# Kernel optimization log

Hardware: AMD Instinct MI355X
Metric: run time of the kernel (lower is better)

## Reference

```python
import jax, jax.numpy as jnp
import numpy as np

B, H, W, C, FD, HID = 64, 128, 128, 10, 32, 64
OFFSETS = [(-1,-1),(-1,0),(-1,1),(0,-1),(0,1),(1,-1),(1,0),(1,1)]

def setup_inputs() -> dict:
    key = jax.random.key(0)
    ks = jax.random.split(key, 13)
    s = lambda n: 1.0 / np.sqrt(n)
    return {
        "beliefs": jax.random.normal(ks[0], (B, H, W, C), jnp.float32),
        "constraints": jax.random.uniform(ks[1], (B, H, W, 8, 3), jnp.float32),
        "filename_embed": jax.random.normal(ks[2], (B, FD), jnp.float32),
        # message_net: Linear(2C+3+FD -> HID), ReLU, Linear(HID -> C)
        "mw1": jax.random.uniform(ks[3], (2*C+3+FD, HID), jnp.float32, -s(2*C+3+FD), s(2*C+3+FD)),
        "mb1": jax.random.uniform(ks[4], (HID,), jnp.float32, -s(2*C+3+FD), s(2*C+3+FD)),
        "mw2": jax.random.uniform(ks[5], (HID, C), jnp.float32, -s(HID), s(HID)),
        "mb2": jax.random.uniform(ks[6], (C,), jnp.float32, -s(HID), s(HID)),
        # update_net: Linear(2C -> HID), ReLU, Linear(HID -> C)
        "uw1": jax.random.uniform(ks[7], (2*C, HID), jnp.float32, -s(2*C), s(2*C)),
        "ub1": jax.random.uniform(ks[8], (HID,), jnp.float32, -s(2*C), s(2*C)),
        "uw2": jax.random.uniform(ks[9], (HID, C), jnp.float32, -s(HID), s(HID)),
        "ub2": jax.random.uniform(ks[10], (C,), jnp.float32, -s(HID), s(HID)),
        "gamma": jnp.ones((C,), jnp.float32),
        "beta": jnp.zeros((C,), jnp.float32),
    }

def reference(beliefs, constraints, filename_embed, mw1, mb1, mw2, mb2, uw1, ub1, uw2, ub2, gamma, beta):
    b, h, w, c = beliefs.shape
    # replicate-pad spatial dims (matches F.pad mode='replicate')
    bp = jnp.pad(beliefs, ((0,0),(1,1),(1,1),(0,0)), mode='edge')
    # gather 8 neighbors -> [B,H,W,8,C]
    neigh = jnp.stack([bp[:, 1+dy:1+dy+h, 1+dx:1+dx+w, :] for dy, dx in OFFSETS], axis=3)
    self_b = jnp.broadcast_to(beliefs[:, :, :, None, :], (b, h, w, 8, c))
    fn = jnp.broadcast_to(filename_embed[:, None, None, None, :], (b, h, w, 8, filename_embed.shape[-1]))
    msg_in = jnp.concatenate([self_b, neigh, constraints, fn], axis=-1)  # [B,H,W,8,2C+3+FD]
    msgs = jax.nn.relu(msg_in @ mw1 + mb1) @ mw2 + mb2                   # [B,H,W,8,C]
    agg = msgs.mean(axis=3)                                              # [B,H,W,C]
    upd_in = jnp.concatenate([beliefs, agg], axis=-1)
    upd = jax.nn.relu(upd_in @ uw1 + ub1) @ uw2 + ub2
    x = beliefs + 0.5 * upd
    mu = x.mean(-1, keepdims=True)
    var = ((x - mu) ** 2).mean(-1, keepdims=True)
    return (x - mu) * jax.lax.rsqrt(var + 1e-5) * gamma + beta
```

## Files before the change

kernel.cpp:

```cpp
#include <hip/hip_runtime.h>
#include <hip/hip_bf16.h>

typedef unsigned int u32;
typedef _Float16 h2 __attribute__((ext_vector_type(2)));

#define TILE 16
#define HALO 18
#define NPIX (HALO*HALO)

#define W_SELF   0
#define W_NBW    320
#define W_WC     640
#define W_MW2    736
#define W_UB1    1056
#define W_UW1    1088
#define W_UW2    1728
#define WS_W     2048
#define WS_SCAL  4096
#define WS_DWORDS 4136

__device__ __forceinline__ h2 pkrtz(float a, float b) {
    return __builtin_bit_cast(h2, __builtin_amdgcn_cvt_pkrtz(a, b));
}
__device__ __forceinline__ float dot2f(h2 a, h2 b, float c) {
#if __has_builtin(__builtin_amdgcn_fdot2)
    return __builtin_amdgcn_fdot2(__builtin_bit_cast(__attribute__((ext_vector_type(2))) __fp16, a),
                                  __builtin_bit_cast(__attribute__((ext_vector_type(2))) __fp16, b),
                                  c, false);
#else
    return c + (float)a.x * (float)b.x + (float)a.y * (float)b.y;
#endif
}
__device__ __forceinline__ h2 relu2(h2 v) {
    h2 z = (h2)(_Float16)0;
#if __has_builtin(__builtin_elementwise_max)
    return __builtin_elementwise_max(v, z);
#else
    h2 r;
    r.x = v.x > (_Float16)0 ? v.x : (_Float16)0;
    r.y = v.y > (_Float16)0 ? v.y : (_Float16)0;
    return r;
#endif
}

__global__ __launch_bounds__(64) void prep_kernel(
    const float* __restrict__ fn,  const float* __restrict__ mw1, const float* __restrict__ mb1,
    const float* __restrict__ mw2, const float* __restrict__ mb2, const float* __restrict__ uw1,
    const float* __restrict__ ub1, const float* __restrict__ uw2, const float* __restrict__ ub2,
    const float* __restrict__ gam, const float* __restrict__ bet, u32* __restrict__ ws)
{
    const int b = blockIdx.x, t = threadIdx.x;
    h2* wh = (h2*)ws;
    if (t < 32) {
        float a0 = mb1[2*t], a1 = mb1[2*t+1];
        for (int f = 0; f < 32; f++) {
            float fv = fn[b*32 + f];
            a0 += fv * mw1[(23+f)*64 + 2*t];
            a1 += fv * mw1[(23+f)*64 + 2*t+1];
        }
        wh[b*32 + t] = pkrtz(a0, a1);
    }
    if (b == 0) {
        for (int i = t; i < 2048; i += 64) {
            float a, c; int j;
            if      (i < 320)  { int cc = i>>5,  hp = i&31;  a = mw1[cc*64 + 2*hp];       c = mw1[cc*64 + 2*hp+1]; }
            else if (i < 640)  { j = i-320;  int q = j>>6, hh = j&63; a = mw1[(10+2*q)*64 + hh]; c = mw1[(11+2*q)*64 + hh]; }
            else if (i < 736)  { j = i-640;  int r = j>>5, hp = j&31; a = mw1[(20+r)*64 + 2*hp]; c = mw1[(20+r)*64 + 2*hp+1]; }
            else if (i < 1056) { j = i-736;  int cc = j>>5, hp = j&31; a = mw2[(2*hp)*10 + cc];  c = mw2[(2*hp+1)*10 + cc]; }
            else if (i < 1088) { j = i-1056; a = ub1[2*j]; c = ub1[2*j+1]; }
            else if (i < 1728) { j = i-1088; int cc = j>>5, hp = j&31; a = uw1[cc*64 + 2*hp];    c = uw1[cc*64 + 2*hp+1]; }
            else               { j = i-1728; int cc = j>>5, hp = j&31; a = uw2[(2*hp)*10 + cc];  c = uw2[(2*hp+1)*10 + cc]; }
            wh[WS_W + i] = pkrtz(a, c);
        }
        if (t < 40) {
            float v;
            if      (t < 10) v = mb2[t];
            else if (t < 20) v = ub2[t-10];
            else if (t < 30) v = gam[t-20];
            else             v = bet[t-30];
            ((float*)ws)[WS_SCAL + t] = v;
        }
    }
}

__global__ __launch_bounds__(256, 3) void mp_kernel(
    const float* __restrict__ beliefs, const float* __restrict__ cons,
    const u32* __restrict__ ws, float* __restrict__ out)
{
    __shared__ h2 bel_s[NPIX*5];
    __shared__ h2 nbp_s[32*NPIX];

    const int tid = threadIdx.x;
    const int b = blockIdx.z, y0 = blockIdx.y*TILE, x0 = blockIdx.x*TILE;

    const h2* Wfnb = (const h2*)ws;
    const h2* W    = ((const h2*)ws) + WS_W;
    const float* SC = ((const float*)ws) + WS_SCAL;

    for (int i = tid; i < NPIX*5; i += 256) {
        int p = i/5, q = i - p*5;
        int py = p/HALO, px = p - py*HALO;
        int gy = y0-1+py; gy = gy<0?0:(gy>127?127:gy);
        int gx = x0-1+px; gx = gx<0?0:(gx>127?127:gx);
        const float2 v = *(const float2*)(beliefs + (size_t)((b*128+gy)*128+gx)*10 + 2*q);
        bel_s[i] = pkrtz(v.x, v.y);
    }
    __syncthreads();

    for (int p = tid; p < NPIX; p += 256) {
        h2 bc[5];
        #pragma unroll
        for (int q = 0; q < 5; q++) bc[q] = bel_s[p*5 + q];
        #pragma unroll 4
        for (int hp = 0; hp < 32; hp++) {
            float a0 = 0.f, a1 = 0.f;
            #pragma unroll
            for (int q = 0; q < 5; q++) {
                a0 = dot2f(bc[q], W[W_NBW + q*64 + 2*hp],     a0);
                a1 = dot2f(bc[q], W[W_NBW + q*64 + 2*hp + 1], a1);
            }
            nbp_s[hp*NPIX + p] = pkrtz(a0, a1);
        }
    }
    __syncthreads();

    const int tx = tid & 15, ty = tid >> 4;
    const int pc = (ty+1)*HALO + (tx+1);
    const size_t gpix = (size_t)((b*128 + (y0+ty))*128 + (x0+tx));

    float bel[10]; h2 beld[10];
    {
        const float2* bp = (const float2*)(beliefs + gpix*10);
        #pragma unroll
        for (int q = 0; q < 5; q++) {
            float2 v = bp[q];
            bel[2*q] = v.x; bel[2*q+1] = v.y;
            beld[2*q]   = pkrtz(v.x, v.x);
            beld[2*q+1] = pkrtz(v.y, v.y);
        }
    }
    h2 cond[24];
    {
        const float4* cp = (const float4*)(cons + gpix*24);
        #pragma unroll
        for (int r = 0; r < 6; r++) {
            float4 v = cp[r];
            cond[4*r+0] = pkrtz(v.x, v.x);
            cond[4*r+1] = pkrtz(v.y, v.y);
            cond[4*r+2] = pkrtz(v.z, v.z);
            cond[4*r+3] = pkrtz(v.w, v.w);
        }
    }

    float acc2[10];
    #pragma unroll
    for (int c = 0; c < 10; c++) acc2[c] = 0.f;

    #pragma unroll 4
    for (int hp = 0; hp < 32; hp++) {
        h2 t01 = Wfnb[b*32 + hp];
        #pragma unroll
        for (int c = 0; c < 10; c++) t01 = beld[c]*W[W_SELF + c*32 + hp] + t01;
        const h2 wc0 = W[W_WC + hp], wc1 = W[W_WC + 32 + hp], wc2 = W[W_WC + 64 + hp];
        const h2* nbb = nbp_s + hp*NPIX + pc - 19;
        h2 s01 = (h2)(_Float16)0;
        #pragma unroll
        for (int k = 0; k < 8; k++) {
            const int doff[8] = {0,1,2,18,20,36,37,38};
            h2 v = t01 + nbb[doff[k]];
            v = cond[k*3+0]*wc0 + v;
            v = cond[k*3+1]*wc1 + v;
            v = cond[k*3+2]*wc2 + v;
            s01 += relu2(v);
        }
        #pragma unroll
        for (int c = 0; c < 10; c++) acc2[c] = dot2f(s01, W[W_MW2 + c*32 + hp], acc2[c]);
    }

    h2 aggd[10];
    #pragma unroll
    for (int c = 0; c < 10; c++) {
        float a = acc2[c]*0.125f + SC[c];
        aggd[c] = pkrtz(a, a);
    }

    float od[10];
    #pragma unroll
    for (int c = 0; c < 10; c++) od[c] = 0.f;

    #pragma unroll 4
    for (int hp = 0; hp < 32; hp++) {
        h2 u01 = W[W_UB1 + hp];
        #pragma unroll
        for (int c = 0; c < 10; c++) u01 = beld[c]*W[W_UW1 + c*32 + hp] + u01;
        #pragma unroll
        for (int c = 0; c < 10; c++) u01 = aggd[c]*W[W_UW1 + (10+c)*32 + hp] + u01;
        u01 = relu2(u01);
        #pragma unroll
        for (int c = 0; c < 10; c++) od[c] = dot2f(u01, W[W_UW2 + c*32 + hp], od[c]);
    }

    float x[10], mu = 0.f;
    #pragma unroll
    for (int c = 0; c < 10; c++) { x[c] = bel[c] + 0.5f*(od[c] + SC[10+c]); mu += x[c]; }
    mu *= 0.1f;
    float var = 0.f;
    #pragma unroll
    for (int c = 0; c < 10; c++) { float d = x[c] - mu; var += d*d; }
    var *= 0.1f;
    const float rs = rsqrtf(var + 1e-5f);

    float2* op = (float2*)(out + gpix*10);
    #pragma unroll
    for (int q = 0; q < 5; q++) {
        float2 r;
        r.x = (x[2*q]   - mu)*rs*SC[20+2*q]   + SC[30+2*q];
        r.y = (x[2*q+1] - mu)*rs*SC[20+2*q+1] + SC[30+2*q+1];
        op[q] = r;
    }
}

__device__ __forceinline__ float bf_lo(u32 v) { return __uint_as_float(v << 16); }
__device__ __forceinline__ float bf_hi(u32 v) { return __uint_as_float(v & 0xffff0000u); }
__device__ __forceinline__ u32 f2bf(float f) {
    u32 u = __float_as_uint(f);
    return (u + 0x7fffu + ((u >> 16) & 1u)) >> 16;
}
__device__ __forceinline__ u32 pack2(float a, float b) { return f2bf(a) | (f2bf(b) << 16); }
__device__ __forceinline__ u32 fpair(const float* a, int pi) { return pack2(a[2*pi], a[2*pi+1]); }

#define FW_MW2 736
#define FW_MB2 1056
#define FW_UW1 1061
#define FW_UB1 1701
#define FW_UW2 1733
#define FW_UB2 2053
#define FW_GAM 2058
#define FW_BET 2063
#define FW_TOT 2068

__global__ __launch_bounds__(256) void fallback_kernel(
    const float* __restrict__ beliefs, const float* __restrict__ cons, const float* __restrict__ fn,
    const float* __restrict__ mw1, const float* __restrict__ mb1, const float* __restrict__ mw2,
    const float* __restrict__ mb2, const float* __restrict__ uw1, const float* __restrict__ ub1,
    const float* __restrict__ uw2, const float* __restrict__ ub2, const float* __restrict__ gam,
    const float* __restrict__ bet, float* __restrict__ out)
{
    __shared__ float bel_s[NPIX*10];
    __shared__ u32   nbp_s[32*NPIX];
    __shared__ u32   w_s[FW_TOT];
    __shared__ float fnb_s[64];

    const int tid = threadIdx.x;
    const int b  = blockIdx.z;
    const int y0 = blockIdx.y * TILE;
    const int x0 = blockIdx.x * TILE;

    for (int i = tid; i < FW_TOT; i += 256) {
        u32 v;
        if      (i < 736)  v = fpair(mw1, i);
        else if (i < 1056) v = fpair(mw2, i - 736);
        else if (i < 1061) v = fpair(mb2, i - 1056);
        else if (i < 1701) v = fpair(uw1, i - 1061);
        else if (i < 1733) v = fpair(ub1, i - 1701);
        else if (i < 2053) v = fpair(uw2, i - 1733);
        else if (i < 2058) v = fpair(ub2, i - 2053);
        else if (i < 2063) v = fpair(gam, i - 2058);
        else               v = fpair(bet, i - 2063);
        w_s[i] = v;
    }
    if (tid < 64) {
        float acc = mb1[tid];
        #pragma unroll 8
        for (int f = 0; f < 32; f++)
            acc += fn[b*32 + f] * mw1[(23 + f)*64 + tid];
        fnb_s[tid] = acc;
    }
    for (int idx = tid; idx < NPIX*10; idx += 256) {
        int p = idx/10, c = idx - p*10;
        int py = p/HALO, px = p - py*HALO;
        int gy = y0-1+py; gy = gy<0?0:(gy>127?127:gy);
        int gx = x0-1+px; gx = gx<0?0:(gx>127?127:gx);
        bel_s[idx] = beliefs[((size_t)(b*128+gy)*128+gx)*10 + c];
    }
    __syncthreads();

    for (int p = tid; p < NPIX; p += 256) {
        float bl[10];
        #pragma unroll
        for (int c = 0; c < 10; c++) bl[c] = bel_s[p*10 + c];
        #pragma unroll 4
        for (int hp = 0; hp < 32; hp++) {
            float t0 = 0.f, t1 = 0.f;
            #pragma unroll
            for (int c = 0; c < 10; c++) {
                u32 wv = w_s[(10 + c)*32 + hp];
                t0 += bl[c] * bf_lo(wv);
                t1 += bl[c] * bf_hi(wv);
            }
            nbp_s[hp*NPIX + p] = pack2(t0, t1);
        }
    }
    __syncthreads();

    const int tx = tid & 15, ty = tid >> 4;
    const int pc = (ty + 1)*HALO + (tx + 1);
    float bel[10];
    #pragma unroll
    for (int c = 0; c < 10; c++) bel[c] = bel_s[pc*10 + c];
    const size_t gpix = (size_t)(b*128 + (y0 + ty))*128 + (x0 + tx);
    float con[24];
    #pragma unroll
    for (int j = 0; j < 24; j++) con[j] = cons[gpix*24 + j];

    float acc2[10];
    #pragma unroll
    for (int c = 0; c < 10; c++) acc2[c] = 0.f;

    #pragma unroll 2
    for (int hp = 0; hp < 32; hp++) {
        const int h0 = 2*hp, h1 = h0 + 1;
        float t0 = fnb_s[h0], t1 = fnb_s[h1];
        #pragma unroll
        for (int c = 0; c < 10; c++) {
            u32 wv = w_s[c*32 + hp];
            t0 += bel[c] * bf_lo(wv);
            t1 += bel[c] * bf_hi(wv);
        }
        const u32 wc0 = w_s[20*32 + hp], wc1 = w_s[21*32 + hp], wc2 = w_s[22*32 + hp];
        const u32* nbb = nbp_s + hp*NPIX + pc - 19;
        float s0 = 0.f, s1 = 0.f;
        #pragma unroll
        for (int k = 0; k < 8; k++) {
            const int doff[8] = { 0, 1, 2, 18, 20, 36, 37, 38 };
            u32 nv = nbb[doff[k]];
            float c0 = con[k*3], c1 = con[k*3+1], c2 = con[k*3+2];
            float v0 = t0 + bf_lo(nv) + c0*bf_lo(wc0) + c1*bf_lo(wc1) + c2*bf_lo(wc2);
            float v1 = t1 + bf_hi(nv) + c0*bf_hi(wc0) + c1*bf_hi(wc1) + c2*bf_hi(wc2);
            s0 += fmaxf(v0, 0.f);
            s1 += fmaxf(v1, 0.f);
        }
        #pragma unroll
        for (int cq = 0; cq < 5; cq++) {
            u32 a0 = w_s[FW_MW2 + h0*5 + cq];
            u32 a1 = w_s[FW_MW2 + h1*5 + cq];
            acc2[2*cq]   += s0*bf_lo(a0) + s1*bf_lo(a1);
            acc2[2*cq+1] += s0*bf_hi(a0) + s1*bf_hi(a1);
        }
    }

    float agg[10];
    #pragma unroll
    for (int cq = 0; cq < 5; cq++) {
        u32 bp = w_s[FW_MB2 + cq];
        agg[2*cq]   = acc2[2*cq]  *0.125f + bf_lo(bp);
        agg[2*cq+1] = acc2[2*cq+1]*0.125f + bf_hi(bp);
    }

    float od[10];
    #pragma unroll
    for (int c = 0; c < 10; c++) od[c] = 0.f;
    #pragma unroll 2
    for (int hp = 0; hp < 32; hp++) {
        u32 ubp = w_s[FW_UB1 + hp];
        float u0 = bf_lo(ubp), u1 = bf_hi(ubp);
        #pragma unroll
        for (int c = 0; c < 10; c++) {
            u32 wv = w_s[FW_UW1 + c*32 + hp];
            u0 += bel[c] * bf_lo(wv);
            u1 += bel[c] * bf_hi(wv);
        }
        #pragma unroll
        for (int c = 0; c < 10; c++) {
            u32 wv = w_s[FW_UW1 + (10 + c)*32 + hp];
            u0 += agg[c] * bf_lo(wv);
            u1 += agg[c] * bf_hi(wv);
        }
        u0 = fmaxf(u0, 0.f); u1 = fmaxf(u1, 0.f);
        const int h0 = 2*hp, h1 = h0 + 1;
        #pragma unroll
        for (int cq = 0; cq < 5; cq++) {
            u32 a0 = w_s[FW_UW2 + h0*5 + cq];
            u32 a1 = w_s[FW_UW2 + h1*5 + cq];
            od[2*cq]   += u0*bf_lo(a0) + u1*bf_lo(a1);
            od[2*cq+1] += u0*bf_hi(a0) + u1*bf_hi(a1);
        }
    }

    float x[10], mu = 0.f;
    #pragma unroll
    for (int cq = 0; cq < 5; cq++) {
        u32 bp = w_s[FW_UB2 + cq];
        x[2*cq]   = bel[2*cq]   + 0.5f*(od[2*cq]   + bf_lo(bp));
        x[2*cq+1] = bel[2*cq+1] + 0.5f*(od[2*cq+1] + bf_hi(bp));
        mu += x[2*cq] + x[2*cq+1];
    }
    mu *= 0.1f;
    float var = 0.f;
    #pragma unroll
    for (int c = 0; c < 10; c++) { float d = x[c] - mu; var += d*d; }
    var *= 0.1f;
    const float rs = rsqrtf(var + 1e-5f);

    float2* op = reinterpret_cast<float2*>(out + gpix*10);
    #pragma unroll
    for (int q = 0; q < 5; q++) {
        u32 gp = w_s[FW_GAM + q], bq = w_s[FW_BET + q];
        float2 r;
        r.x = (x[2*q]   - mu)*rs*bf_lo(gp) + bf_lo(bq);
        r.y = (x[2*q+1] - mu)*rs*bf_hi(gp) + bf_hi(bq);
        op[q] = r;
    }
}

extern "C" void kernel_launch(void* const* d_in, const int* in_sizes, int n_in,
                              void* d_out, int out_size, void* d_ws, size_t ws_size,
                              hipStream_t stream) {
    (void)in_sizes; (void)n_in; (void)out_size;
    const float* beliefs = (const float*)d_in[0];
    const float* cons    = (const float*)d_in[1];
    const float* fn      = (const float*)d_in[2];
    const float* mw1     = (const float*)d_in[3];
    const float* mb1     = (const float*)d_in[4];
    const float* mw2     = (const float*)d_in[5];
    const float* mb2     = (const float*)d_in[6];
    const float* uw1     = (const float*)d_in[7];
    const float* ub1     = (const float*)d_in[8];
    const float* uw2     = (const float*)d_in[9];
    const float* ub2     = (const float*)d_in[10];
    const float* gam     = (const float*)d_in[11];
    const float* bet     = (const float*)d_in[12];
    float* outp = (float*)d_out;

    if (ws_size >= (size_t)WS_DWORDS*4) {
        prep_kernel<<<dim3(64), dim3(64), 0, stream>>>(
            fn, mw1, mb1, mw2, mb2, uw1, ub1, uw2, ub2, gam, bet, (u32*)d_ws);
        mp_kernel<<<dim3(8, 8, 64), dim3(256), 0, stream>>>(
            beliefs, cons, (const u32*)d_ws, outp);
    } else {
        fallback_kernel<<<dim3(8, 8, 64), dim3(256), 0, stream>>>(
            beliefs, cons, fn, mw1, mb1, mw2, mb2, uw1, ub1, uw2, ub2, gam, bet, outp);
    }
}
```

Baseline: 320.2 us.

## Store neighbor projections pixel-major and process hidden units in chunks of four

Moves the neighbor-projection shared buffer from hidden-major to pixel-major layout with a padded stride of 36, so each neighbor read fetches four packed hidden pairs in one 128-bit LDS load. The message loop is restructured to handle four hidden pairs per iteration to match. Multiply-adds now go through explicit packed fp16 FMA helpers so they fuse reliably. The larger shared buffer (36 instead of 32 entries per pixel) and higher register use could reduce occupancy, and the stride choice may introduce bank conflicts.

Result: no change. 318.3 us (-0.6%).

```diff
diff --git a/kernel.cpp b/kernel.cpp
--- a/kernel.cpp
+++ b/kernel.cpp
@@ -7,6 +7,7 @@
 #define TILE 16
 #define HALO 18
 #define NPIX (HALO*HALO)
+#define NBSTRIDE 36
 
 #define W_SELF   0
 #define W_NBW    320
@@ -22,13 +23,19 @@
 __device__ __forceinline__ h2 pkrtz(float a, float b) {
     return __builtin_bit_cast(h2, __builtin_amdgcn_cvt_pkrtz(a, b));
 }
+#if __has_builtin(__builtin_elementwise_fma)
+__device__ __forceinline__ h2 pkfma(h2 a, h2 b, h2 c) { return __builtin_elementwise_fma(a, b, c); }
+#else
+extern "C" __device__ h2 __ocml_fma_2f16(h2, h2, h2);
+__device__ __forceinline__ h2 pkfma(h2 a, h2 b, h2 c) { return __ocml_fma_2f16(a, b, c); }
+#endif
 __device__ __forceinline__ float dot2f(h2 a, h2 b, float c) {
 #if __has_builtin(__builtin_amdgcn_fdot2)
     return __builtin_amdgcn_fdot2(__builtin_bit_cast(__attribute__((ext_vector_type(2))) __fp16, a),
                                   __builtin_bit_cast(__attribute__((ext_vector_type(2))) __fp16, b),
                                   c, false);
 #else
-    return c + (float)a.x * (float)b.x + (float)a.y * (float)b.y;
+    return fmaf((float)a.x, (float)b.x, fmaf((float)a.y, (float)b.y, c));
 #endif
 }
 __device__ __forceinline__ h2 relu2(h2 v) {
@@ -42,6 +49,7 @@
     return r;
 #endif
 }
+__device__ __forceinline__ h2 h2cast(u32 v) { return __builtin_bit_cast(h2, v); }
 
 __global__ __launch_bounds__(64) void prep_kernel(
     const float* __restrict__ fn,  const float* __restrict__ mw1, const float* __restrict__ mb1,
@@ -88,7 +96,7 @@
     const u32* __restrict__ ws, float* __restrict__ out)
 {
     __shared__ h2 bel_s[NPIX*5];
-    __shared__ h2 nbp_s[32*NPIX];
+    __shared__ __align__(16) u32 nbp_u[NPIX*NBSTRIDE];
 
     const int tid = threadIdx.x;
     const int b = blockIdx.z, y0 = blockIdx.y*TILE, x0 = blockIdx.x*TILE;
@@ -119,7 +127,7 @@
                 a0 = dot2f(bc[q], W[W_NBW + q*64 + 2*hp],     a0);
                 a1 = dot2f(bc[q], W[W_NBW + q*64 + 2*hp + 1], a1);
             }
-            nbp_s[hp*NPIX + p] = pkrtz(a0, a1);
+            nbp_u[p*NBSTRIDE + hp] = __builtin_bit_cast(u32, pkrtz(a0, a1));
         }
     }
     __syncthreads();
@@ -127,6 +135,13 @@
     const int tx = tid & 15, ty = tid >> 4;
     const int pc = (ty+1)*HALO + (tx+1);
     const size_t gpix = (size_t)((b*128 + (y0+ty))*128 + (x0+tx));
+
+    int p36[8];
+    {
+        const int doff[8] = {-19,-18,-17,-1,1,17,18,19};
+        #pragma unroll
+        for (int k = 0; k < 8; k++) p36[k] = (pc + doff[k]) * NBSTRIDE;
+    }
 
     float bel[10]; h2 beld[10];
     {
@@ -156,25 +171,45 @@
     #pragma unroll
     for (int c = 0; c < 10; c++) acc2[c] = 0.f;
 
-    #pragma unroll 4
-    for (int hp = 0; hp < 32; hp++) {
-        h2 t01 = Wfnb[b*32 + hp];
-        #pragma unroll
-        for (int c = 0; c < 10; c++) t01 = beld[c]*W[W_SELF + c*32 + hp] + t01;
-        const h2 wc0 = W[W_WC + hp], wc1 = W[W_WC + 32 + hp], wc2 = W[W_WC + 64 + hp];
-        const h2* nbb = nbp_s + hp*NPIX + pc - 19;
-        h2 s01 = (h2)(_Float16)0;
+    #pragma unroll 2
+    for (int ch = 0; ch < 8; ch++) {
+        const int hb = 4*ch;
+        h2 t01[4], s01[4];
+        #pragma unroll
+        for (int j = 0; j < 4; j++) { t01[j] = Wfnb[b*32 + hb + j]; s01[j] = (h2)(_Float16)0; }
+        #pragma unroll
+        for (int c = 0; c < 10; c++) {
+            #pragma unroll
+            for (int j = 0; j < 4; j++)
+                t01[j] = pkfma(beld[c], W[W_SELF + c*32 + hb + j], t01[j]);
+        }
+        h2 wc0[4], wc1[4], wc2[4];
+        #pragma unroll
+        for (int j = 0; j < 4; j++) {
+            wc0[j] = W[W_WC      + hb + j];
+            wc1[j] = W[W_WC + 32 + hb + j];
+            wc2[j] = W[W_WC + 64 + hb + j];
+        }
         #pragma unroll
         for (int k = 0; k < 8; k++) {
-            const int doff[8] = {0,1,2,18,20,36,37,38};
-            h2 v = t01 + nbb[doff[k]];
-            v = cond[k*3+0]*wc0 + v;
-            v = cond[k*3+1]*wc1 + v;
-            v = cond[k*3+2]*wc2 + v;
-            s01 += relu2(v);
-        }
-        #pragma unroll
-        for (int c = 0; c < 10; c++) acc2[c] = dot2f(s01, W[W_MW2 + c*32 + hp], acc2[c]);
+            const uint4 nv = *(const uint4*)(nbp_u + p36[k] + hb);
+            const h2 nb[4] = { h2cast(nv.x), h2cast(nv.y), h2cast(nv.z), h2cast(nv.w) };
+            const h2 c0 = cond[k*3+0], c1 = cond[k*3+1], c2 = cond[k*3+2];
+            #pragma unroll
+            for (int j = 0; j < 4; j++) {
+                h2 v = t01[j] + nb[j];
+                v = pkfma(c0, wc0[j], v);
+                v = pkfma(c1, wc1[j], v);
+                v = pkfma(c2, wc2[j], v);
+                s01[j] += relu2(v);
+            }
+        }
+        #pragma unroll
+        for (int c = 0; c < 10; c++) {
+            #pragma unroll
+            for (int j = 0; j < 4; j++)
+                acc2[c] = dot2f(s01[j], W[W_MW2 + c*32 + hb + j], acc2[c]);
+        }
     }
 
     h2 aggd[10];
@@ -192,9 +227,9 @@
     for (int hp = 0; hp < 32; hp++) {
         h2 u01 = W[W_UB1 + hp];
         #pragma unroll
-        for (int c = 0; c < 10; c++) u01 = beld[c]*W[W_UW1 + c*32 + hp] + u01;
-        #pragma unroll
-        for (int c = 0; c < 10; c++) u01 = aggd[c]*W[W_UW1 + (10+c)*32 + hp] + u01;
+        for (int c = 0; c < 10; c++) u01 = pkfma(beld[c], W[W_UW1 + c*32 + hp], u01);
+        #pragma unroll
+        for (int c = 0; c < 10; c++) u01 = pkfma(aggd[c], W[W_UW1 + (10+c)*32 + hp], u01);
         u01 = relu2(u01);
         #pragma unroll
         for (int c = 0; c < 10; c++) od[c] = dot2f(u01, W[W_UW2 + c*32 + hp], od[c]);
```
